# Kernel optimization log

Hardware: AMD Instinct MI355X
Metric: run time of the kernel (lower is better)

Reference implementation:

```python
import jax, jax.numpy as jnp
import numpy as np

B, S, D, H = 8, 1024, 1024, 16
DK = D // H
EPS = 1e-5

def _layernorm(x, w, b):
    mu = jnp.mean(x, axis=-1, keepdims=True)
    var = jnp.mean((x - mu) ** 2, axis=-1, keepdims=True)
    return (x - mu) * jax.lax.rsqrt(var + EPS) * w + b

def setup_inputs() -> dict:
    key = jax.random.key(0)
    ks = jax.random.split(key, 12)
    x = jax.random.normal(ks[0], (B, S, D), dtype=jnp.float32)
    batch_lengths = jax.random.randint(ks[1], (B,), S // 2, S + 1, dtype=jnp.int32)
    sc = 1.0 / np.sqrt(D)
    Wq = jax.random.normal(ks[2], (H, D, DK), dtype=jnp.float32) * sc
    Wk = jax.random.normal(ks[3], (H, D, DK), dtype=jnp.float32) * sc
    Wv = jax.random.normal(ks[4], (H, D, DK), dtype=jnp.float32) * sc
    fc1_w = jax.random.normal(ks[5], (D, D), dtype=jnp.float32) * sc
    fc1_b = jnp.zeros((D,), dtype=jnp.float32)
    fc2_w = jax.random.normal(ks[6], (D, D), dtype=jnp.float32) * sc
    fc2_b = jnp.zeros((D,), dtype=jnp.float32)
    ln1_w = jnp.ones((D,), dtype=jnp.float32)
    ln1_b = jnp.zeros((D,), dtype=jnp.float32)
    ln2_w = jnp.ones((D,), dtype=jnp.float32)
    ln2_b = jnp.zeros((D,), dtype=jnp.float32)
    return {"x": x, "Wq": Wq, "Wk": Wk, "Wv": Wv, "fc1_w": fc1_w, "fc1_b": fc1_b,
            "fc2_w": fc2_w, "fc2_b": fc2_b, "ln1_w": ln1_w, "ln1_b": ln1_b,
            "ln2_w": ln2_w, "ln2_b": ln2_b, "batch_lengths": batch_lengths, "max_len": S}

def reference(x, Wq, Wk, Wv, fc1_w, fc1_b, fc2_w, fc2_b, ln1_w, ln1_b, ln2_w, ln2_b, batch_lengths, max_len):
    b, s, d = x.shape
    h, _, dk = Wq.shape
    # padding masks: valid positions are t < length
    row = (jnp.arange(s)[None, :] < batch_lengths[:, None]).astype(x.dtype)  # [B,S]
    m = row[:, :, None]                 # [B,S,1], outputMask per-row
    mh = m[:, None]                     # [B,1,S,1]
    # all heads batched: Q,K,V -> [B,H,S,dk], masked like Wq(ctx)*mask etc.
    Q = jnp.einsum('bsd,hde->bhse', x, Wq) * mh
    K = jnp.einsum('bsd,hde->bhse', x, Wk) * mh
    V = jnp.einsum('bsd,hde->bhse', x, Wv) * mh
    energy = jnp.einsum('bhqe,bhke->bhqk', Q, K)
    # attnMask: key columns beyond length -> -inf
    key_valid = row[:, None, None, :] > 0
    energy = jnp.where(key_valid, energy, -jnp.inf)
    score = jax.nn.softmax(energy / jnp.sqrt(jnp.asarray(dk, x.dtype)), axis=-1)
    z = jnp.einsum('bhqk,bhke->bhqe', score, V)           # [B,H,S,dk]
    z = z.transpose(0, 2, 1, 3).reshape(b, s, d) * m      # concat heads, mask
    x1 = _layernorm(x + z, ln1_w, ln1_b)
    ff = jax.nn.relu(x1 @ fc1_w + fc1_b) * m
    ff = (ff @ fc2_w + fc2_b) * m
    return _layernorm(x1 + ff, ln2_w, ln2_b)
```

## Files before the change

### kernel.cpp

```cpp
#include <hip/hip_runtime.h>
#include <math.h>

#define B_ 8
#define S_ 1024
#define D_ 1024
#define H_ 16
#define DK_ 64
#define EPS_ 1e-5f

typedef __bf16 bf16_t;
typedef __bf16 bf16x8 __attribute__((ext_vector_type(8)));
typedef __bf16 bf16x4v __attribute__((ext_vector_type(4)));
typedef float  f32x4  __attribute__((ext_vector_type(4)));

__device__ __forceinline__ void gld16(const void* g, void* l) {
    __builtin_amdgcn_global_load_lds(
        (const __attribute__((address_space(1))) void*)g,
        (__attribute__((address_space(3))) void*)l, 16, 0, 0);
}

__global__ __launch_bounds__(256)
void prep(const float* __restrict__ x,
          const float* __restrict__ Wq, const float* __restrict__ Wk,
          const float* __restrict__ Wv, const float* __restrict__ W1,
          const float* __restrict__ W2, bf16_t* __restrict__ xb,
          bf16_t* __restrict__ WtQKV, bf16_t* __restrict__ Wt1,
          bf16_t* __restrict__ Wt2)
{
    __shared__ float tile[64][65];
    const int tid = threadIdx.x;
    const int z = blockIdx.z;

    if (z >= 5) {
        const int blk = (z - 5) * 256 + blockIdx.y * 16 + blockIdx.x;
        const int i = (blk * 256 + tid) * 4;
        const float4 v = *(const float4*)(x + i);
        bf16x4v o = { (bf16_t)v.x, (bf16_t)v.y, (bf16_t)v.z, (bf16_t)v.w };
        *(bf16x4v*)(xb + i) = o;
        return;
    }

    const int n0 = blockIdx.x * 64, k0 = blockIdx.y * 64;
    const int col = tid & 63, r0 = tid >> 6;
    const float* src = (z == 0) ? Wq : (z == 1) ? Wk : (z == 2) ? Wv
                     : (z == 3) ? W1 : W2;
    #pragma unroll
    for (int i = 0; i < 16; i++) {
        const int row = r0 + i * 4;
        float v;
        if (z < 3)
            v = src[((size_t)(n0 >> 6) << 16) + (size_t)(k0 + row) * 64 + col];
        else
            v = src[(size_t)(k0 + row) * D_ + n0 + col];
        tile[row][col] = v;
    }
    __syncthreads();
    bf16_t* dst = (z < 3) ? (WtQKV + (size_t)z * D_ * D_)
                : (z == 3) ? Wt1 : Wt2;
    #pragma unroll
    for (int i = 0; i < 16; i++) {
        const int nr = r0 + i * 4;
        dst[(size_t)(n0 + nr) * D_ + k0 + col] = (bf16_t)tile[col][nr];
    }
}

template<int EPI, int BN, typename OUT>
__global__ __launch_bounds__(512, 2)
void gemm8(const bf16_t* __restrict__ A, const bf16_t* __restrict__ Bw,
           const float* __restrict__ bias, const int* __restrict__ lens,
           OUT* __restrict__ C, int M, int N, int K)
{
    constexpr int NSB = BN / 64;
    constexpr int WN  = BN / 4;
    constexpr int NJ  = WN / 16;

    __shared__ __align__(16) bf16_t As[2][256 * 64];
    __shared__ __align__(16) bf16_t Bs[2][BN * 64];

    const int tid  = threadIdx.x;
    const int lane = tid & 63;
    const int w    = tid >> 6;
    const int quad = lane >> 4, l16 = lane & 15;
    const int wm = w & 1, wn = w >> 1;
    const int sw8 = l16 & 7;

    const int nwg  = gridDim.x * gridDim.y;
    const int orig = blockIdx.y * gridDim.x + blockIdx.x;
    const int swz  = (orig & 7) * (nwg >> 3) + (orig >> 3);
    const int bn = (swz % gridDim.x) * BN;
    const int bm = (swz / gridDim.x) * 256;

    const int rS  = tid >> 3;
    const int cS  = ((tid & 7) ^ (rS & 7)) << 3;
    const int dOf = w * 64 * 16;

    f32x4 acc[8][NJ];
    #pragma unroll
    for (int i = 0; i < 8; i++)
        #pragma unroll
        for (int j = 0; j < NJ; j++)
            #pragma unroll
            for (int r = 0; r < 4; r++) acc[i][j][r] = 0.f;

#define STAGE(buf_, kt_) { \
    _Pragma("unroll") \
    for (int s_ = 0; s_ < 4; s_++) \
        gld16(A + (size_t)(bm + s_ * 64 + rS) * K + (kt_) * 64 + cS, \
              (char*)As[buf_] + s_ * 8192 + dOf); \
    _Pragma("unroll") \
    for (int s_ = 0; s_ < NSB; s_++) \
        gld16(Bw + (size_t)(bn + s_ * 64 + rS) * K + (kt_) * 64 + cS, \
              (char*)Bs[buf_] + s_ * 8192 + dOf); }
#define RD_A(dst, qm_, i_, kh_) \
    dst = *(const bf16x8*)&Ac[(wm * 128 + (qm_) * 64 + (i_) * 16 + l16) * 64 + ((((kh_) * 4 + quad) ^ sw8) << 3)];
#define RD_B(dst, qn_, j_, kh_) \
    dst = *(const bf16x8*)&Bc[(wn * WN + (qn_) * 32 + (j_) * 16 + l16) * 64 + ((((kh_) * 4 + quad) ^ sw8) << 3)];
#define MM(QI, QJ, AF, BF) \
    _Pragma("unroll") \
    for (int kh_ = 0; kh_ < 2; kh_++) \
        _Pragma("unroll") \
        for (int i_ = 0; i_ < 4; i_++) \
            _Pragma("unroll") \
            for (int j_ = 0; j_ < 2; j_++) \
                acc[(QI) * 4 + i_][(QJ) * 2 + j_] = __builtin_amdgcn_mfma_f32_16x16x32_bf16( \
                    AF[i_][kh_], BF[j_][kh_], acc[(QI) * 4 + i_][(QJ) * 2 + j_], 0, 0, 0);

    const int NKT = K >> 6;

    STAGE(0, 0);

    for (int t = 0; t < NKT; ++t) {
        const int cb = t & 1, nb = cb ^ 1;
        const int ktn = (t + 1 < NKT) ? t + 1 : t;
        const bf16_t* Ac = As[cb];
        const bf16_t* Bc = Bs[cb];

        STAGE(nb, ktn);
        if constexpr (BN == 256)
            asm volatile("s_waitcnt vmcnt(8)" ::: "memory");
        else
            asm volatile("s_waitcnt vmcnt(6)" ::: "memory");
        __builtin_amdgcn_sched_barrier(0);
        __builtin_amdgcn_s_barrier();
        __builtin_amdgcn_sched_barrier(0);

        bf16x8 fa[4][2], fb[2][2];
        #pragma unroll
        for (int i = 0; i < 4; i++) { RD_A(fa[i][0], 0, i, 0); RD_A(fa[i][1], 0, i, 1); }
        #pragma unroll
        for (int j = 0; j < 2; j++) { RD_B(fb[j][0], 0, j, 0); RD_B(fb[j][1], 0, j, 1); }
        __builtin_amdgcn_s_setprio(1);
        MM(0, 0, fa, fb);
        __builtin_amdgcn_s_setprio(0);

        if constexpr (BN == 256) {
            bf16x8 gb[2][2];
            #pragma unroll
            for (int j = 0; j < 2; j++) { RD_B(gb[j][0], 1, j, 0); RD_B(gb[j][1], 1, j, 1); }
            __builtin_amdgcn_s_setprio(1);
            MM(0, 1, fa, gb);
            __builtin_amdgcn_s_setprio(0);
            bf16x8 ga[4][2];
            #pragma unroll
            for (int i = 0; i < 4; i++) { RD_A(ga[i][0], 1, i, 0); RD_A(ga[i][1], 1, i, 1); }
            __builtin_amdgcn_s_setprio(1);
            MM(1, 1, ga, gb);
            MM(1, 0, ga, fb);
            __builtin_amdgcn_s_setprio(0);
        } else {
            bf16x8 ga[4][2];
            #pragma unroll
            for (int i = 0; i < 4; i++) { RD_A(ga[i][0], 1, i, 0); RD_A(ga[i][1], 1, i, 1); }
            __builtin_amdgcn_s_setprio(1);
            MM(1, 0, ga, fb);
            __builtin_amdgcn_s_setprio(0);
        }

        __builtin_amdgcn_sched_barrier(0);
        __builtin_amdgcn_s_barrier();
    }

#undef STAGE
#undef RD_A
#undef RD_B
#undef MM

    #pragma unroll
    for (int ii = 0; ii < 8; ii++) {
        #pragma unroll
        for (int r = 0; r < 4; r++) {
            const int m = bm + wm * 128 + (ii >> 2) * 64 + (ii & 3) * 16 + quad * 4 + r;
            float keep = 1.f;
            if (EPI != 0) {
                const int s = m & (S_ - 1);
                const int bb = m >> 10;
                keep = (s < lens[bb]) ? 1.f : 0.f;
            }
            #pragma unroll
            for (int jj = 0; jj < NJ; jj++) {
                const int n = bn + wn * WN + (jj >> 1) * 32 + (jj & 1) * 16 + l16;
                float v = acc[ii][jj][r];
                if (EPI != 0) {
                    v += bias[n];
                    if (EPI == 1) v = fmaxf(v, 0.f);
                    v *= keep;
                }
                C[(size_t)m * N + n] = (OUT)v;
            }
        }
    }
}

__global__ __launch_bounds__(256, 3)
void attn_mfma(const bf16_t* __restrict__ QKV, const int* __restrict__ lens,
               bf16_t* __restrict__ Z)
{
    __shared__ __align__(16) bf16_t Ks[2][64][64];
    __shared__ __align__(16) bf16_t Vt[2][64][72];
    __shared__ __align__(16) bf16_t Ps[64][72];

    const int tid  = threadIdx.x;
    const int lane = tid & 63;
    const int w    = tid >> 6;
    const int quad = lane >> 4;
    const int l16  = lane & 15;
    const int id   = blockIdx.x;
    const int b    = id & 7;
    const int h    = (id >> 3) & 15;
    const int qt   = id >> 7;
    const int len  = lens[b];
    const int qbase = qt * 64;
    const bf16_t* Qp = QKV + (size_t)b * S_ * 3072 + (size_t)h * 64;
    const bf16_t* Kp = Qp + 1024;
    const bf16_t* Vp = Qp + 2048;
    const size_t zbase = (size_t)b * S_ * D_ + (size_t)h * 64;

    if (qbase >= len) {
        const int r = tid >> 2, c0 = (tid & 3) * 16;
        bf16_t* zp = Z + zbase + (size_t)(qbase + r) * D_ + c0;
        uint4 zz = {0u, 0u, 0u, 0u};
        *(uint4*)zp = zz;
        *(uint4*)(zp + 8) = zz;
        return;
    }

    const int qrow = qbase + w * 16 + l16;
    const bf16x8 bq0 = *(const bf16x8*)(Qp + (size_t)qrow * 3072 + quad * 8);
    const bf16x8 bq1 = *(const bf16x8*)(Qp + (size_t)qrow * 3072 + 32 + quad * 8);

    const int kr0  = tid >> 3;
    const int kpos = tid & 7;
    const int kc0  = (kpos ^ (kr0 & 7)) << 3;
    const int kc1  = (kpos ^ ((kr0 + 32) & 7)) << 3;

    const int vr  = tid >> 2;
    const int vc0 = (tid & 3) * 16;
    const int vp  = vr ^ ((tid & 3) << 4);

    f32x4 o[4];
    #pragma unroll
    for (int dm = 0; dm < 4; dm++)
        #pragma unroll
        for (int r = 0; r < 4; r++) o[dm][r] = 0.f;
    float l_q = 0.f;

    const int ntiles = (len + 63) >> 6;

    gld16(Kp + (size_t)kr0 * 3072 + kc0,
          (char*)&Ks[0][0][0] + (size_t)(w * 64) * 16);
    gld16(Kp + (size_t)(kr0 + 32) * 3072 + kc1,
          (char*)&Ks[0][0][0] + (size_t)(256 + w * 64) * 16);
    bf16x8 vcur0 = *(const bf16x8*)(Vp + (size_t)vr * 3072 + vc0);
    bf16x8 vcur1 = *(const bf16x8*)(Vp + (size_t)vr * 3072 + vc0 + 8);
    __syncthreads();

    for (int t = 0; t < ntiles; t++) {
        const int k0 = t * 64;
        const int cb = t & 1, nb = (t + 1) & 1;
        const int kn0 = (t + 1 < ntiles ? t + 1 : t) * 64;

        gld16(Kp + (size_t)(kn0 + kr0) * 3072 + kc0,
              (char*)&Ks[nb][0][0] + (size_t)(w * 64) * 16);
        gld16(Kp + (size_t)(kn0 + kr0 + 32) * 3072 + kc1,
              (char*)&Ks[nb][0][0] + (size_t)(256 + w * 64) * 16);
        const bf16_t* vsrc = Vp + (size_t)(kn0 + vr) * 3072 + vc0;
        const bf16x8 vn0 = *(const bf16x8*)vsrc;
        const bf16x8 vn1 = *(const bf16x8*)(vsrc + 8);
        __builtin_amdgcn_sched_barrier(0);

        #pragma unroll
        for (int kt = 0; kt < 4; kt++) {
            const int r = kt * 16 + l16;
            const bf16x8 ak0 = *(const bf16x8*)&Ks[cb][r][(quad ^ (l16 & 7)) << 3];
            const bf16x8 ak1 = *(const bf16x8*)&Ks[cb][r][((4 + quad) ^ (l16 & 7)) << 3];
            f32x4 z4 = {0.f, 0.f, 0.f, 0.f};
            z4 = __builtin_amdgcn_mfma_f32_16x16x32_bf16(ak0, bq0, z4, 0, 0, 0);
            const f32x4 sfv = __builtin_amdgcn_mfma_f32_16x16x32_bf16(ak1, bq1, z4, 0, 0, 0);
            bf16x4v pk;
            #pragma unroll
            for (int r2 = 0; r2 < 4; r2++) {
                const int key = k0 + kt * 16 + quad * 4 + r2;
                float p = __expf(sfv[r2] * 0.125f);
                p = (key < len) ? p : 0.f;
                l_q += p;
                pk[r2] = (bf16_t)p;
            }
            *(bf16x4v*)&Ps[w * 16 + l16][kt * 16 + quad * 4] = pk;
        }

        #pragma unroll
        for (int i = 0; i < 8; i++) Vt[cb][vc0 + i][vp] = vcur0[i];
        #pragma unroll
        for (int i = 0; i < 8; i++) Vt[cb][vc0 + 8 + i][vp] = vcur1[i];
        vcur0 = vn0;
        vcur1 = vn1;
        __syncthreads();

        const bf16x8 bp0 = *(const bf16x8*)&Ps[w * 16 + l16][quad * 8];
        const bf16x8 bp1 = *(const bf16x8*)&Ps[w * 16 + l16][32 + quad * 8];
        #pragma unroll
        for (int dm = 0; dm < 4; dm++) {
            const bf16x8 av0 = *(const bf16x8*)&Vt[cb][dm * 16 + l16][(quad * 8) ^ (dm * 16)];
            const bf16x8 av1 = *(const bf16x8*)&Vt[cb][dm * 16 + l16][(32 + quad * 8) ^ (dm * 16)];
            o[dm] = __builtin_amdgcn_mfma_f32_16x16x32_bf16(av0, bp0, o[dm], 0, 0, 0);
            o[dm] = __builtin_amdgcn_mfma_f32_16x16x32_bf16(av1, bp1, o[dm], 0, 0, 0);
        }
    }

    l_q += __shfl_xor(l_q, 16);
    l_q += __shfl_xor(l_q, 32);
    const int qg = qbase + w * 16 + l16;
    const float inv = (qg < len) ? 1.f / l_q : 0.f;
    bf16_t* zrow = Z + zbase + (size_t)qg * D_;
    #pragma unroll
    for (int dm = 0; dm < 4; dm++) {
        bf16x4v st;
        #pragma unroll
        for (int r = 0; r < 4; r++) st[r] = (bf16_t)(o[dm][r] * inv);
        *(bf16x4v*)(zrow + dm * 16 + quad * 4) = st;
    }
}

__device__ __forceinline__ void ln_core(float vx, float vy, float vz, float vw,
                                        int tid, float& mean, float& rstd)
{
    __shared__ float red[8];
    float s = vx + vy + vz + vw;
    #pragma unroll
    for (int off = 32; off; off >>= 1) s += __shfl_xor(s, off, 64);
    const int wv = tid >> 6, lane = tid & 63;
    if (lane == 0) red[wv] = s;
    __syncthreads();
    mean = (red[0] + red[1] + red[2] + red[3]) * (1.f / D_);
    const float dx = vx - mean, dy = vy - mean, dz = vz - mean, dw = vw - mean;
    float s2 = dx * dx + dy * dy + dz * dz + dw * dw;
    #pragma unroll
    for (int off = 32; off; off >>= 1) s2 += __shfl_xor(s2, off, 64);
    if (lane == 0) red[4 + wv] = s2;
    __syncthreads();
    rstd = rsqrtf((red[4] + red[5] + red[6] + red[7]) * (1.f / D_) + EPS_);
}

__global__ __launch_bounds__(256)
void add_ln1(const float* __restrict__ X, const bf16_t* __restrict__ Y,
             const float* __restrict__ g, const float* __restrict__ beta,
             bf16_t* __restrict__ out)
{
    const int row = blockIdx.x, tid = threadIdx.x;
    const float4 xv = ((const float4*)(X + (size_t)row * D_))[tid];
    const bf16x4v yv = *(const bf16x4v*)(Y + (size_t)row * D_ + tid * 4);
    const float vx = xv.x + (float)yv[0], vy = xv.y + (float)yv[1];
    const float vz = xv.z + (float)yv[2], vw = xv.w + (float)yv[3];
    float mean, rstd;
    ln_core(vx, vy, vz, vw, tid, mean, rstd);
    const float4 gv = ((const float4*)g)[tid];
    const float4 bv = ((const float4*)beta)[tid];
    bf16x4v o;
    o[0] = (bf16_t)((vx - mean) * rstd * gv.x + bv.x);
    o[1] = (bf16_t)((vy - mean) * rstd * gv.y + bv.y);
    o[2] = (bf16_t)((vz - mean) * rstd * gv.z + bv.z);
    o[3] = (bf16_t)((vw - mean) * rstd * gv.w + bv.w);
    *(bf16x4v*)(out + (size_t)row * D_ + tid * 4) = o;
}

__global__ __launch_bounds__(256)
void add_ln2(const bf16_t* __restrict__ X, const float* __restrict__ Y,
             const float* __restrict__ g, const float* __restrict__ beta,
             float* __restrict__ out)
{
    const int row = blockIdx.x, tid = threadIdx.x;
    const bf16x4v xv = *(const bf16x4v*)(X + (size_t)row * D_ + tid * 4);
    const float4 yv = ((const float4*)(Y + (size_t)row * D_))[tid];
    const float vx = (float)xv[0] + yv.x, vy = (float)xv[1] + yv.y;
    const float vz = (float)xv[2] + yv.z, vw = (float)xv[3] + yv.w;
    float mean, rstd;
    ln_core(vx, vy, vz, vw, tid, mean, rstd);
    const float4 gv = ((const float4*)g)[tid];
    const float4 bv = ((const float4*)beta)[tid];
    float4 o;
    o.x = (vx - mean) * rstd * gv.x + bv.x;
    o.y = (vy - mean) * rstd * gv.y + bv.y;
    o.z = (vz - mean) * rstd * gv.z + bv.z;
    o.w = (vw - mean) * rstd * gv.w + bv.w;
    ((float4*)(out + (size_t)row * D_))[tid] = o;
}

extern "C" void kernel_launch(void* const* d_in, const int* in_sizes, int n_in,
                              void* d_out, int out_size, void* d_ws, size_t ws_size,
                              hipStream_t stream)
{
    const float* x    = (const float*)d_in[0];
    const float* Wq   = (const float*)d_in[1];
    const float* Wk   = (const float*)d_in[2];
    const float* Wv   = (const float*)d_in[3];
    const float* fc1w = (const float*)d_in[4];
    const float* fc1b = (const float*)d_in[5];
    const float* fc2w = (const float*)d_in[6];
    const float* fc2b = (const float*)d_in[7];
    const float* ln1w = (const float*)d_in[8];
    const float* ln1b = (const float*)d_in[9];
    const float* ln2w = (const float*)d_in[10];
    const float* ln2b = (const float*)d_in[11];
    const int*   lens = (const int*)d_in[12];
    float* out = (float*)d_out;

    char* ws = (char*)d_ws;
    const size_t MB = 1024 * 1024;
    bf16_t* QKVb  = (bf16_t*)(ws);
    bf16_t* Zb    = (bf16_t*)(ws + 48 * MB);
    bf16_t* X1b   = (bf16_t*)(ws + 80 * MB);
    bf16_t* xb    = (bf16_t*)(ws + 96 * MB);
    bf16_t* H1b   = (bf16_t*)(ws + 96 * MB);
    float*  FF    = (float*)(ws + 48 * MB);
    bf16_t* WtQKV = (bf16_t*)(ws + 112 * MB);
    bf16_t* Wt1   = (bf16_t*)(ws + 118 * MB);
    bf16_t* Wt2   = (bf16_t*)(ws + 120 * MB);

    const int M = B_ * S_;

    prep<<<dim3(16, 16, 37), 256, 0, stream>>>(x, Wq, Wk, Wv, fc1w, fc2w,
                                               xb, WtQKV, Wt1, Wt2);

    gemm8<0, 256, bf16_t><<<dim3(3072 / 256, M / 256), 512, 0, stream>>>(
        xb, WtQKV, nullptr, nullptr, QKVb, M, 3072, D_);

    attn_mfma<<<dim3(2048), 256, 0, stream>>>(QKVb, lens, Zb);

    add_ln1<<<M, 256, 0, stream>>>(x, Zb, ln1w, ln1b, X1b);

    gemm8<1, 128, bf16_t><<<dim3(D_ / 128, M / 256), 512, 0, stream>>>(
        X1b, Wt1, fc1b, lens, H1b, M, D_, D_);
    gemm8<2, 128, float><<<dim3(D_ / 128, M / 256), 512, 0, stream>>>(
        H1b, Wt2, fc2b, lens, FF, M, D_, D_);

    add_ln2<<<M, 256, 0, stream>>>(X1b, FF, ln2w, ln2b, out);
}
```

Baseline: 330.0 us.

## Interleave global-to-LDS staging with MFMA quadrants in 8-wave GEMM loop

Restructures the GEMM main loop into four quadrant phases. The next tile's global-to-LDS loads are split and issued between the MFMA phases rather than all at the start of each iteration, with partial vmcnt waits and extra barriers. The aim is to spread memory traffic across the compute and overlap it better, in the style of the hipBLASLt ping-pong schedule. This adds more barriers per iteration and depends on careful vmcnt accounting; the BN=128 path now also computes four quadrants with half-width B fragments.

```diff
diff --git a/kernel.cpp b/kernel.cpp
--- a/kernel.cpp
+++ b/kernel.cpp
@@ -70,9 +70,9 @@
            const float* __restrict__ bias, const int* __restrict__ lens,
            OUT* __restrict__ C, int M, int N, int K)
 {
-    constexpr int NSB = BN / 64;
     constexpr int WN  = BN / 4;
     constexpr int NJ  = WN / 16;
+    constexpr int NJB = NJ / 2;
 
     __shared__ __align__(16) bf16_t As[2][256 * 64];
     __shared__ __align__(16) bf16_t Bs[2][BN * 64];
@@ -92,7 +92,7 @@
 
     const int rS  = tid >> 3;
     const int cS  = ((tid & 7) ^ (rS & 7)) << 3;
-    const int dOf = w * 64 * 16;
+    const int dOf = w * 1024;
 
     f32x4 acc[8][NJ];
     #pragma unroll
@@ -102,32 +102,37 @@
             #pragma unroll
             for (int r = 0; r < 4; r++) acc[i][j][r] = 0.f;
 
-#define STAGE(buf_, kt_) { \
-    _Pragma("unroll") \
-    for (int s_ = 0; s_ < 4; s_++) \
-        gld16(A + (size_t)(bm + s_ * 64 + rS) * K + (kt_) * 64 + cS, \
-              (char*)As[buf_] + s_ * 8192 + dOf); \
-    _Pragma("unroll") \
-    for (int s_ = 0; s_ < NSB; s_++) \
-        gld16(Bw + (size_t)(bn + s_ * 64 + rS) * K + (kt_) * 64 + cS, \
-              (char*)Bs[buf_] + s_ * 8192 + dOf); }
+#define SA(s_, b_, kt_) \
+    gld16(A + (size_t)(bm + (s_) * 64 + rS) * K + (kt_) * 64 + cS, \
+          (char*)As[b_] + (s_) * 8192 + dOf);
+#define SBW(s_, b_, kt_) \
+    gld16(Bw + (size_t)(bn + (s_) * 64 + rS) * K + (kt_) * 64 + cS, \
+          (char*)Bs[b_] + (s_) * 8192 + dOf);
 #define RD_A(dst, qm_, i_, kh_) \
     dst = *(const bf16x8*)&Ac[(wm * 128 + (qm_) * 64 + (i_) * 16 + l16) * 64 + ((((kh_) * 4 + quad) ^ sw8) << 3)];
 #define RD_B(dst, qn_, j_, kh_) \
-    dst = *(const bf16x8*)&Bc[(wn * WN + (qn_) * 32 + (j_) * 16 + l16) * 64 + ((((kh_) * 4 + quad) ^ sw8) << 3)];
+    dst = *(const bf16x8*)&Bc[(wn * WN + (qn_) * (WN / 2) + (j_) * 16 + l16) * 64 + ((((kh_) * 4 + quad) ^ sw8) << 3)];
 #define MM(QI, QJ, AF, BF) \
     _Pragma("unroll") \
     for (int kh_ = 0; kh_ < 2; kh_++) \
         _Pragma("unroll") \
         for (int i_ = 0; i_ < 4; i_++) \
             _Pragma("unroll") \
-            for (int j_ = 0; j_ < 2; j_++) \
-                acc[(QI) * 4 + i_][(QJ) * 2 + j_] = __builtin_amdgcn_mfma_f32_16x16x32_bf16( \
-                    AF[i_][kh_], BF[j_][kh_], acc[(QI) * 4 + i_][(QJ) * 2 + j_], 0, 0, 0);
+            for (int j_ = 0; j_ < NJB; j_++) \
+                acc[(QI) * 4 + i_][(QJ) * NJB + j_] = __builtin_amdgcn_mfma_f32_16x16x32_bf16( \
+                    AF[i_][kh_], BF[j_][kh_], acc[(QI) * 4 + i_][(QJ) * NJB + j_], 0, 0, 0);
+#define SB0() __builtin_amdgcn_sched_barrier(0)
+#define BARR() __builtin_amdgcn_s_barrier()
+#define LGK0() asm volatile("s_waitcnt lgkmcnt(0)" ::: "memory")
 
     const int NKT = K >> 6;
 
-    STAGE(0, 0);
+    SBW(0, 0, 0); SBW(1, 0, 0);
+    if constexpr (BN == 256) { SBW(2, 0, 0); SBW(3, 0, 0); }
+    SA(0, 0, 0); SA(2, 0, 0);
+    SA(1, 0, 0); SA(3, 0, 0);
+    asm volatile("s_waitcnt vmcnt(2)" ::: "memory");
+    BARR();
 
     for (int t = 0; t < NKT; ++t) {
         const int cb = t & 1, nb = cb ^ 1;
@@ -135,55 +140,59 @@
         const bf16_t* Ac = As[cb];
         const bf16_t* Bc = Bs[cb];
 
-        STAGE(nb, ktn);
-        if constexpr (BN == 256)
-            asm volatile("s_waitcnt vmcnt(8)" ::: "memory");
-        else
-            asm volatile("s_waitcnt vmcnt(6)" ::: "memory");
-        __builtin_amdgcn_sched_barrier(0);
-        __builtin_amdgcn_s_barrier();
-        __builtin_amdgcn_sched_barrier(0);
-
-        bf16x8 fa[4][2], fb[2][2];
+        bf16x8 fa[4][2], fb[NJB][2];
         #pragma unroll
         for (int i = 0; i < 4; i++) { RD_A(fa[i][0], 0, i, 0); RD_A(fa[i][1], 0, i, 1); }
         #pragma unroll
-        for (int j = 0; j < 2; j++) { RD_B(fb[j][0], 0, j, 0); RD_B(fb[j][1], 0, j, 1); }
+        for (int j = 0; j < NJB; j++) { RD_B(fb[j][0], 0, j, 0); RD_B(fb[j][1], 0, j, 1); }
+        SBW(0, nb, ktn); SBW(1, nb, ktn);
+        SB0(); BARR(); LGK0(); SB0();
         __builtin_amdgcn_s_setprio(1);
         MM(0, 0, fa, fb);
         __builtin_amdgcn_s_setprio(0);
-
-        if constexpr (BN == 256) {
-            bf16x8 gb[2][2];
-            #pragma unroll
-            for (int j = 0; j < 2; j++) { RD_B(gb[j][0], 1, j, 0); RD_B(gb[j][1], 1, j, 1); }
-            __builtin_amdgcn_s_setprio(1);
-            MM(0, 1, fa, gb);
-            __builtin_amdgcn_s_setprio(0);
-            bf16x8 ga[4][2];
-            #pragma unroll
-            for (int i = 0; i < 4; i++) { RD_A(ga[i][0], 1, i, 0); RD_A(ga[i][1], 1, i, 1); }
-            __builtin_amdgcn_s_setprio(1);
-            MM(1, 1, ga, gb);
-            MM(1, 0, ga, fb);
-            __builtin_amdgcn_s_setprio(0);
-        } else {
-            bf16x8 ga[4][2];
-            #pragma unroll
-            for (int i = 0; i < 4; i++) { RD_A(ga[i][0], 1, i, 0); RD_A(ga[i][1], 1, i, 1); }
-            __builtin_amdgcn_s_setprio(1);
-            MM(1, 0, ga, fb);
-            __builtin_amdgcn_s_setprio(0);
-        }
-
-        __builtin_amdgcn_sched_barrier(0);
-        __builtin_amdgcn_s_barrier();
-    }
-
-#undef STAGE
+        SB0(); BARR();
+
+        bf16x8 gb[NJB][2];
+        #pragma unroll
+        for (int j = 0; j < NJB; j++) { RD_B(gb[j][0], 1, j, 0); RD_B(gb[j][1], 1, j, 1); }
+        if constexpr (BN == 256) { SBW(2, nb, ktn); SBW(3, nb, ktn); }
+        SA(0, nb, ktn); SA(2, nb, ktn);
+        if constexpr (BN == 256)
+            asm volatile("s_waitcnt vmcnt(6)" ::: "memory");
+        else
+            asm volatile("s_waitcnt vmcnt(4)" ::: "memory");
+        SB0(); BARR(); LGK0(); SB0();
+        __builtin_amdgcn_s_setprio(1);
+        MM(0, 1, fa, gb);
+        __builtin_amdgcn_s_setprio(0);
+        SB0(); BARR();
+
+        bf16x8 ga[4][2];
+        #pragma unroll
+        for (int i = 0; i < 4; i++) { RD_A(ga[i][0], 1, i, 0); RD_A(ga[i][1], 1, i, 1); }
+        SB0(); BARR(); LGK0(); SB0();
+        __builtin_amdgcn_s_setprio(1);
+        MM(1, 1, ga, gb);
+        __builtin_amdgcn_s_setprio(0);
+        SB0(); BARR();
+
+        SA(1, nb, ktn); SA(3, nb, ktn);
+        asm volatile("s_waitcnt vmcnt(2)" ::: "memory");
+        SB0(); BARR(); SB0();
+        __builtin_amdgcn_s_setprio(1);
+        MM(1, 0, ga, fb);
+        __builtin_amdgcn_s_setprio(0);
+        SB0(); BARR();
+    }
+
+#undef SA
+#undef SBW
 #undef RD_A
 #undef RD_B
 #undef MM
+#undef SB0
+#undef BARR
+#undef LGK0
 
     #pragma unroll
     for (int ii = 0; ii < 8; ii++) {
```

New measurement: 327.0 us. About the same (-0.9%).
